# Optimization experiments

Measured on AMD Instinct MI355X. Metric: run time of the kernel, lower is better.

Reference implementation:

```python
import jax, jax.numpy as jnp
import numpy as np

N_NODES = 100000
N_EDGES = 1600000
IN_DIM = 512
HID_DIM = 64
N_CLASSES = 10
N_GRAPHS = 64


def setup_inputs() -> dict:
    key = jax.random.key(0)
    ks = jax.random.split(key, 8)
    x = jax.random.normal(ks[0], (N_NODES, IN_DIM), dtype=jnp.float32)
    edge_src = jax.random.randint(ks[1], (N_EDGES,), 0, N_NODES)
    edge_dst = jax.random.randint(ks[2], (N_EDGES,), 0, N_NODES)
    node2graph = jnp.sort(jax.random.randint(ks[3], (N_NODES,), 0, N_GRAPHS))
    W1 = jax.random.normal(ks[4], (IN_DIM, HID_DIM), dtype=jnp.float32) * (1.0 / np.sqrt(IN_DIM))
    b1 = jnp.zeros((HID_DIM,), dtype=jnp.float32)
    W2 = jax.random.normal(ks[5], (HID_DIM, N_CLASSES), dtype=jnp.float32) * (1.0 / np.sqrt(HID_DIM))
    b2 = jnp.zeros((N_CLASSES,), dtype=jnp.float32)
    return {"x": x, "edge_src": edge_src, "edge_dst": edge_dst,
            "node2graph": node2graph, "n_graphs": N_GRAPHS,
            "W1": W1, "b1": b1, "W2": W2, "b2": b2}


def reference(x, edge_src, edge_dst, node2graph, n_graphs, W1, b1, W2, b2):
    n = x.shape[0]
    ones_e = jnp.ones(edge_src.shape[0], dtype=x.dtype)
    # DGL GraphConv norm='both': src scaled by out-deg^-1/2, dst by in-deg^-1/2 (degrees clamped to 1)
    out_deg = jax.ops.segment_sum(ones_e, edge_src, num_segments=n)
    in_deg = jax.ops.segment_sum(ones_e, edge_dst, num_segments=n)
    src_norm = jax.lax.rsqrt(jnp.maximum(out_deg, 1.0))  # [N]
    dst_norm = jax.lax.rsqrt(jnp.maximum(in_deg, 1.0))   # [N]

    def graph_conv(h, W, b):
        h = (h * src_norm[:, None]) @ W                       # [N, out]
        agg = jax.ops.segment_sum(h[edge_src], edge_dst, num_segments=n)  # SpMM
        return agg * dst_norm[:, None] + b

    h = jax.nn.relu(graph_conv(x, W1, b1))
    h = graph_conv(h, W2, b2)
    # dgl.mean_nodes: per-graph mean over nodes
    counts = jax.ops.segment_sum(jnp.ones(n, dtype=x.dtype), node2graph, num_segments=n_graphs)
    sums = jax.ops.segment_sum(h, node2graph, num_segments=n_graphs)
    return sums / jnp.maximum(counts, 1.0)[:, None]
```

## Files before the change

kernel.cpp:

```cpp
#include <hip/hip_runtime.h>

#define NN 100000
#define NE 1600000
#define NG 64
#define BPB  50
#define NBUK 2000
#define NBUK2 2048
#define ECAP 1120
#define GPART 256
#define PREPB 128
#define ZEROB 3
#define GSTB ((NN+255)/256)

using bf16x8 = __attribute__((ext_vector_type(8))) short;
using f32x4  = __attribute__((ext_vector_type(4))) float;

__device__ inline unsigned short f2bf(float f){
    union { float f; unsigned u; } v; v.f = f;
    unsigned r = (v.u + 0x7FFFu + ((v.u >> 16) & 1u)) >> 16;
    return (unsigned short)r;
}

__device__ inline bf16x8 cvt8(float4 a, float4 b){
    union { unsigned u[4]; bf16x8 v; } r;
    asm("v_cvt_pk_bf16_f32 %0, %1, %2" : "=v"(r.u[0]) : "v"(a.x), "v"(a.y));
    asm("v_cvt_pk_bf16_f32 %0, %1, %2" : "=v"(r.u[1]) : "v"(a.z), "v"(a.w));
    asm("v_cvt_pk_bf16_f32 %0, %1, %2" : "=v"(r.u[2]) : "v"(b.x), "v"(b.y));
    asm("v_cvt_pk_bf16_f32 %0, %1, %2" : "=v"(r.u[3]) : "v"(b.z), "v"(b.w));
    return r.v;
}

__global__ __launch_bounds__(256) void k_start(const int* __restrict__ src, const int* __restrict__ dst,
                                               int* __restrict__ cntD, int* __restrict__ cntS, int E,
                                               const float* __restrict__ W1, short* __restrict__ Wb,
                                               float* __restrict__ pooled,
                                               const int* __restrict__ n2g, int* __restrict__ gstart, int N){
    __shared__ int hD[NBUK2], hS[NBUK2];
    int bid = blockIdx.x;
    int tid = threadIdx.x;
    if (bid < GPART){
        for (int i=tid; i<NBUK2; i+=256){ hD[i]=0; hS[i]=0; }
        __syncthreads();
        int chunk = (E + GPART - 1)/GPART;
        int start = bid*chunk;
        int end   = min(E, start + chunk);
        for (int e = start + tid; e < end; e += 256){
            atomicAdd(&hS[src[e]/BPB], 1);
            atomicAdd(&hD[dst[e]/BPB], 1);
        }
        __syncthreads();
        for (int i=tid; i<NBUK2; i+=256){
            cntD[bid*NBUK2 + i] = hD[i];
            cntS[bid*NBUK2 + i] = hS[i];
        }
    } else if (bid < GPART+PREPB){
        int i = (bid-GPART)*256 + tid;
        if (i < 512*64){
            int k = i >> 6, c = i & 63;
            int g = k >> 5, r = k & 31, s = r >> 3, j = r & 7;
            Wb[(((g*4+s)*64 + c) << 3) + j] = (short)f2bf(W1[i]);
        }
    } else if (bid < GPART+PREPB+ZEROB){
        int i = (bid-GPART-PREPB)*256 + tid;
        if (i < NG*10) pooled[i] = 0.f;
    } else {
        int n = (bid-GPART-PREPB-ZEROB)*256 + tid;
        if (n < N){
            int g  = n2g[n];
            int gp = (n == 0) ? -1 : n2g[n-1];
            if (gp != g){
                for (int gg = gp+1; gg <= g; ++gg) gstart[gg] = n;
            }
            if (n == N-1){
                for (int gg = g+1; gg <= NG; ++gg) gstart[gg] = N;
            }
        }
    }
}

__global__ __launch_bounds__(256) void k_scanA(const int* __restrict__ cntD, const int* __restrict__ cntS,
                                               int* __restrict__ totD, int* __restrict__ totS){
    int t = blockIdx.x*256 + threadIdx.x;
    int sD=0, sS=0;
    for (int b=0;b<GPART;b++){ sD += cntD[b*NBUK2+t]; sS += cntS[b*NBUK2+t]; }
    totD[t]=sD; totS[t]=sS;
}

__global__ __launch_bounds__(1024) void k_scanB(const int* __restrict__ totD, const int* __restrict__ totS,
                                                int* __restrict__ bstartD, int* __restrict__ bstartS){
    __shared__ int sd[1024];
    int t = threadIdx.x;
    {
        int v0 = totD[2*t], v1 = totD[2*t+1];
        sd[t] = v0+v1; __syncthreads();
        for (int off=1; off<1024; off<<=1){
            int tv = (t >= off) ? sd[t-off] : 0;
            __syncthreads();
            sd[t] += tv;
            __syncthreads();
        }
        int excl = sd[t] - v0 - v1;
        if (2*t   <= NBUK) bstartD[2*t]   = excl;
        if (2*t+1 <= NBUK) bstartD[2*t+1] = excl + v0;
        __syncthreads();
    }
    {
        int v0 = totS[2*t], v1 = totS[2*t+1];
        sd[t] = v0+v1; __syncthreads();
        for (int off=1; off<1024; off<<=1){
            int tv = (t >= off) ? sd[t-off] : 0;
            __syncthreads();
            sd[t] += tv;
            __syncthreads();
        }
        int excl = sd[t] - v0 - v1;
        if (2*t   <= NBUK) bstartS[2*t]   = excl;
        if (2*t+1 <= NBUK) bstartS[2*t+1] = excl + v0;
    }
}

__global__ __launch_bounds__(256) void k_scanC(int* __restrict__ cntD, int* __restrict__ cntS,
                                               const int* __restrict__ bstartD, const int* __restrict__ bstartS){
    int t = blockIdx.x*256 + threadIdx.x;
    if (t < NBUK){
        int rD = bstartD[t], rS = bstartS[t];
        for (int b=0;b<GPART;b++){
            int idx = b*NBUK2 + t;
            int o = cntD[idx]; cntD[idx] = rD; rD += o;
            o = cntS[idx];     cntS[idx] = rS; rS += o;
        }
    }
}

__global__ __launch_bounds__(256) void k_scatter(const int* __restrict__ src, const int* __restrict__ dst,
                                                 const int* __restrict__ cntD, const int* __restrict__ cntS,
                                                 int* __restrict__ pairs, int* __restrict__ srcl, int E){
    __shared__ unsigned oD[NBUK2], oS[NBUK2];
    for (int i=threadIdx.x; i<NBUK2; i+=256){
        oD[i] = (unsigned)cntD[blockIdx.x*NBUK2 + i];
        oS[i] = (unsigned)cntS[blockIdx.x*NBUK2 + i];
    }
    __syncthreads();
    int chunk = (E + GPART - 1)/GPART;
    int start = blockIdx.x*chunk;
    int end   = min(E, start + chunk);
    for (int e = start + threadIdx.x; e < end; e += 256){
        int s = src[e], d = dst[e];
        int bk = d/BPB;
        unsigned pD = atomicAdd(&oD[bk], 1u);
        pairs[pD] = (s << 6) | (d - bk*BPB);
        unsigned pS = atomicAdd(&oS[s/BPB], 1u);
        srcl[pS] = s;
    }
}

__global__ __launch_bounds__(256) void k_outdeg(const int* __restrict__ srcl, const int* __restrict__ bstartS,
                                                float* __restrict__ sn, int N){
    __shared__ int c[BPB];
    int b = blockIdx.x;
    if (threadIdx.x < BPB) c[threadIdx.x] = 0;
    __syncthreads();
    int s0 = bstartS[b], s1 = bstartS[b+1];
    int base = b*BPB;
    for (int i = s0 + threadIdx.x; i < s1; i += 256)
        atomicAdd(&c[srcl[i] - base], 1);
    __syncthreads();
    int node = base + threadIdx.x;
    if (threadIdx.x < BPB && node < N)
        sn[node] = rsqrtf((float)max(c[threadIdx.x], 1));
}

__global__ __launch_bounds__(256) void k_gemm1(const float* __restrict__ x, const short* __restrict__ Wb,
                                               const float* __restrict__ sn, unsigned short* __restrict__ hb, int N){
    const int lane = threadIdx.x & 63;
    const int wid  = threadIdx.x >> 6;
    const int rowBase = blockIdx.x*128 + wid*32;
    const int mrow = lane & 15;
    const int s    = lane >> 4;

    int rowA = rowBase + mrow;
    int rowB = rowBase + 16 + mrow;
    int rcA = (rowA < N) ? rowA : (N-1);
    int rcB = (rowB < N) ? rowB : (N-1);

    const float4* __restrict__ xv = (const float4*)x;
    const bf16x8* __restrict__ wv = (const bf16x8*)Wb;
    const float4* xrA = xv + (size_t)rcA*128 + s*2;
    const float4* xrB = xv + (size_t)rcB*128 + s*2;

    f32x4 accA0 = {0,0,0,0}, accA1 = {0,0,0,0}, accA2 = {0,0,0,0}, accA3 = {0,0,0,0};
    f32x4 accB0 = {0,0,0,0}, accB1 = {0,0,0,0}, accB2 = {0,0,0,0}, accB3 = {0,0,0,0};

    #pragma unroll 2
    for (int g=0; g<16; g++){
        float4 a0 = xrA[g*8 + 0];
        float4 a1 = xrA[g*8 + 1];
        float4 c0 = xrB[g*8 + 0];
        float4 c1 = xrB[g*8 + 1];
        bf16x8 afA = cvt8(a0, a1);
        bf16x8 afB = cvt8(c0, c1);
        int bbase = (g*4 + s)*64 + mrow;
        bf16x8 b0 = wv[bbase     ];
        bf16x8 b1 = wv[bbase + 16];
        bf16x8 b2 = wv[bbase + 32];
        bf16x8 b3 = wv[bbase + 48];
        accA0 = __builtin_amdgcn_mfma_f32_16x16x32_bf16(afA, b0, accA0, 0, 0, 0);
        accA1 = __builtin_amdgcn_mfma_f32_16x16x32_bf16(afA, b1, accA1, 0, 0, 0);
        accA2 = __builtin_amdgcn_mfma_f32_16x16x32_bf16(afA, b2, accA2, 0, 0, 0);
        accA3 = __builtin_amdgcn_mfma_f32_16x16x32_bf16(afA, b3, accA3, 0, 0, 0);
        accB0 = __builtin_amdgcn_mfma_f32_16x16x32_bf16(afB, b0, accB0, 0, 0, 0);
        accB1 = __builtin_amdgcn_mfma_f32_16x16x32_bf16(afB, b1, accB1, 0, 0, 0);
        accB2 = __builtin_amdgcn_mfma_f32_16x16x32_bf16(afB, b2, accB2, 0, 0, 0);
        accB3 = __builtin_amdgcn_mfma_f32_16x16x32_bf16(afB, b3, accB3, 0, 0, 0);
    }

    #pragma unroll
    for (int q=0; q<4; q++){
        int rr = rowBase + s*4 + q;
        if (rr < N){
            float scale = sn[rr];
            unsigned short* hp = hb + ((size_t)rr<<6) + mrow;
            hp[ 0] = f2bf(accA0[q] * scale);
            hp[16] = f2bf(accA1[q] * scale);
            hp[32] = f2bf(accA2[q] * scale);
            hp[48] = f2bf(accA3[q] * scale);
        }
        int r2 = rowBase + 16 + s*4 + q;
        if (r2 < N){
            float scale = sn[r2];
            unsigned short* hp = hb + ((size_t)r2<<6) + mrow;
            hp[ 0] = f2bf(accB0[q] * scale);
            hp[16] = f2bf(accB1[q] * scale);
            hp[32] = f2bf(accB2[q] * scale);
            hp[48] = f2bf(accB3[q] * scale);
        }
    }
}

__global__ __launch_bounds__(256) void k_agg(const int* __restrict__ pairs, const int* __restrict__ bstartD,
                                             const unsigned short* __restrict__ hb,
                                             const float* __restrict__ sn, const float* __restrict__ b1,
                                             const float* __restrict__ W2,
                                             float* __restrict__ h2, int* __restrict__ gsrc,
                                             int* __restrict__ glh, int N){
    __shared__ int lsrc[ECAP];
    __shared__ int lcnt[BPB];
    __shared__ int lstart[BPB+1];
    __shared__ unsigned lofs[BPB];
    __shared__ __align__(16) float w2t[10][64];
    __shared__ float b1s[64];
    __shared__ __align__(16) float a1s[BPB][68];
    int tid = threadIdx.x;
    if (tid < BPB) lcnt[tid] = 0;
    if (tid < 64)  b1s[tid] = b1[tid];
    for (int i=tid; i<640; i+=256){ int c = i>>6, k = i&63; w2t[c][k] = W2[k*10 + c]; }
    __syncthreads();

    int b = blockIdx.x;
    int nodeBase = b*BPB;
    int eb = bstartD[b], ee = bstartD[b+1];
    int ne = ee - eb;

    for (int i = tid; i < ne; i += 256){
        int pr = pairs[eb + i];
        atomicAdd(&lcnt[pr & 63], 1);
    }
    __syncthreads();
    if (tid < 64){
        int v = (tid < BPB) ? lcnt[tid] : 0;
        int sI = v;
        for (int off=1; off<64; off<<=1){
            int t = __shfl_up(sI, off);
            if (tid >= off) sI += t;
        }
        if (tid < BPB){
            lstart[tid] = sI - v;
            lofs[tid]   = (unsigned)(sI - v);
            if (tid == BPB-1) lstart[BPB] = sI;
        }
    }
    __syncthreads();
    for (int i = tid; i < ne; i += 256){
        int pr = pairs[eb + i];
        unsigned pos = atomicAdd(&lofs[pr & 63], 1u);
        lsrc[pos < ECAP ? pos : ECAP-1] = pr >> 6;
    }
    __syncthreads();

    for (int i = tid; i < ne; i += 256) gsrc[eb + i] = lsrc[i];
    if (tid <= BPB) glh[b*64 + tid] = eb + lstart[tid];

    int lane = tid & 63, wid = tid >> 6;
    int q  = lane >> 4;
    int c4 = lane & 15;

    for (int nl = wid; nl < BPB; nl += 4){
        int node = nodeBase + nl;
        int s0 = lstart[nl];
        int m  = lstart[nl+1] - s0;

        float a0=0.f, a1f=0.f, a2=0.f, a3=0.f;
        int j = 0;
        for (; j + 16 <= m; j += 16){
            int sa = lsrc[s0 + j + q];
            int sb = lsrc[s0 + j + 4 + q];
            int sc = lsrc[s0 + j + 8 + q];
            int sd = lsrc[s0 + j + 12 + q];
            uint2 va = *(const uint2*)(hb + ((size_t)sa<<6) + (c4<<2));
            uint2 vb = *(const uint2*)(hb + ((size_t)sb<<6) + (c4<<2));
            uint2 vc = *(const uint2*)(hb + ((size_t)sc<<6) + (c4<<2));
            uint2 vd = *(const uint2*)(hb + ((size_t)sd<<6) + (c4<<2));
            a0  += __uint_as_float((va.x & 0xffffu) << 16) + __uint_as_float((vb.x & 0xffffu) << 16)
                 + __uint_as_float((vc.x & 0xffffu) << 16) + __uint_as_float((vd.x & 0xffffu) << 16);
            a1f += __uint_as_float(va.x & 0xffff0000u) + __uint_as_float(vb.x & 0xffff0000u)
                 + __uint_as_float(vc.x & 0xffff0000u) + __uint_as_float(vd.x & 0xffff0000u);
            a2  += __uint_as_float((va.y & 0xffffu) << 16) + __uint_as_float((vb.y & 0xffffu) << 16)
                 + __uint_as_float((vc.y & 0xffffu) << 16) + __uint_as_float((vd.y & 0xffffu) << 16);
            a3  += __uint_as_float(va.y & 0xffff0000u) + __uint_as_float(vb.y & 0xffff0000u)
                 + __uint_as_float(vc.y & 0xffff0000u) + __uint_as_float(vd.y & 0xffff0000u);
        }
        for (; j + 8 <= m; j += 8){
            int sa = lsrc[s0 + j + q];
            int sb = lsrc[s0 + j + 4 + q];
            uint2 va = *(const uint2*)(hb + ((size_t)sa<<6) + (c4<<2));
            uint2 vb = *(const uint2*)(hb + ((size_t)sb<<6) + (c4<<2));
            a0  += __uint_as_float((va.x & 0xffffu) << 16) + __uint_as_float((vb.x & 0xffffu) << 16);
            a1f += __uint_as_float(va.x & 0xffff0000u) + __uint_as_float(vb.x & 0xffff0000u);
            a2  += __uint_as_float((va.y & 0xffffu) << 16) + __uint_as_float((vb.y & 0xffffu) << 16);
            a3  += __uint_as_float(va.y & 0xffff0000u) + __uint_as_float(vb.y & 0xffff0000u);
        }
        for (; j < m; j += 4){
            int idx = j + q;
            int idxc = (idx < m) ? idx : (m-1);
            int sa = lsrc[s0 + idxc];
            uint2 va = *(const uint2*)(hb + ((size_t)sa<<6) + (c4<<2));
            if (idx < m){
                a0  += __uint_as_float((va.x & 0xffffu) << 16);
                a1f += __uint_as_float(va.x & 0xffff0000u);
                a2  += __uint_as_float((va.y & 0xffffu) << 16);
                a3  += __uint_as_float(va.y & 0xffff0000u);
            }
        }
        a0  += __shfl_xor(a0, 16);  a0  += __shfl_xor(a0, 32);
        a1f += __shfl_xor(a1f, 16); a1f += __shfl_xor(a1f, 32);
        a2  += __shfl_xor(a2, 16);  a2  += __shfl_xor(a2, 32);
        a3  += __shfl_xor(a3, 16);  a3  += __shfl_xor(a3, 32);

        float dnv = rsqrtf((float)max(m, 1));
        float snv = sn[node];
        float r0 = fmaxf(fmaf(a0,  dnv, b1s[(c4<<2)+0]), 0.f) * snv;
        float r1 = fmaxf(fmaf(a1f, dnv, b1s[(c4<<2)+1]), 0.f) * snv;
        float r2 = fmaxf(fmaf(a2,  dnv, b1s[(c4<<2)+2]), 0.f) * snv;
        float r3 = fmaxf(fmaf(a3,  dnv, b1s[(c4<<2)+3]), 0.f) * snv;
        if (q == 0){
            *(float4*)(&a1s[nl][c4<<2]) = make_float4(r0, r1, r2, r3);
        }
    }
    __syncthreads();

    for (int i = tid; i < BPB*10; i += 256){
        int nl = i / 10;
        int c  = i - nl*10;
        int node = nodeBase + nl;
        if (node < N){
            const float4* ap = (const float4*)(&a1s[nl][0]);
            const float4* wp = (const float4*)(&w2t[c][0]);
            float acc = 0.f;
            #pragma unroll
            for (int p=0;p<16;p++){
                float4 a = ap[p]; float4 w = wp[p];
                acc = fmaf(a.x, w.x, fmaf(a.y, w.y, fmaf(a.z, w.z, fmaf(a.w, w.w, acc))));
            }
            h2[(size_t)node*10 + c] = acc;
        }
    }
}

__global__ __launch_bounds__(256) void k_pool2(const int* __restrict__ gsrc, const int* __restrict__ glh,
                                               const float* __restrict__ h2, const int* __restrict__ n2g,
                                               float* __restrict__ pooled, int N){
    __shared__ float accS[NG*10];
    int tid = threadIdx.x;
    for (int i=tid; i<NG*10; i+=256) accS[i] = 0.f;
    __syncthreads();
    int b = blockIdx.x;
    int nodeBase = b*BPB;
    int lane = tid & 63, wid = tid >> 6;
    int e6 = lane/10, c = lane - e6*10;
    bool active = (lane < 60);

    for (int nl = wid; nl < BPB; nl += 4){
        int node = nodeBase + nl;
        int base = glh[b*64 + nl];
        int m    = glh[b*64 + nl + 1] - base;
        float acc = 0.f;
        for (int j = 0; j < m; j += 6){
            int idx = j + e6;
            int idxc = (idx < m) ? idx : (m-1);
            int srcn = gsrc[base + idxc];
            float v = h2[(size_t)srcn*10 + c];
            if (active && idx < m) acc += v;
        }
        float t0 = __shfl(acc, lane+30); if (lane < 30) acc += t0;
        float t1 = __shfl(acc, lane+10);
        float t2 = __shfl(acc, lane+20);
        if (lane < 10){
            acc += t1 + t2;
            float dnv = rsqrtf((float)max(m, 1));
            int g = n2g[node];
            atomicAdd(&accS[g*10 + lane], dnv*acc);
        }
    }
    __syncthreads();
    int g0 = n2g[nodeBase], g1 = n2g[nodeBase + BPB - 1];
    int lo = g0*10, hi = g1*10 + 10;
    for (int i = lo + tid; i < hi; i += 256)
        atomicAdd(&pooled[i], accS[i]);
}

__global__ void k_out(const float* __restrict__ pooled, const int* __restrict__ gstart,
                      const float* __restrict__ b2, float* __restrict__ out){
    int i = blockIdx.x*blockDim.x + threadIdx.x;
    if (i < NG*10){
        int g = i/10, c = i - g*10;
        float cnt = (float)max(gstart[g+1] - gstart[g], 1);
        out[i] = pooled[i]/cnt + b2[c];
    }
}

extern "C" void kernel_launch(void* const* d_in, const int* in_sizes, int n_in,
                              void* d_out, int out_size, void* d_ws, size_t ws_size,
                              hipStream_t stream) {
    const float* x    = (const float*)d_in[0];
    const int*   esrc = (const int*)d_in[1];
    const int*   edst = (const int*)d_in[2];
    const int*   n2g  = (const int*)d_in[3];
    const float* W1   = (const float*)d_in[5];
    const float* b1   = (const float*)d_in[6];
    const float* W2   = (const float*)d_in[7];
    const float* b2   = (const float*)d_in[8];
    float* out = (float*)d_out;
    const int N = in_sizes[3];
    const int E = in_sizes[1];

    char* ws = (char*)d_ws;
    size_t off = 0;
    auto alloc = [&](size_t bytes) -> void* {
        void* p = ws + off;
        off = (off + bytes + 255) & ~(size_t)255;
        return p;
    };
    float* pooled  = (float*)alloc(NG*10*4);
    int*   cntD    = (int*)alloc((size_t)GPART*NBUK2*4);
    int*   cntS    = (int*)alloc((size_t)GPART*NBUK2*4);
    int*   totD    = (int*)alloc(NBUK2*4);
    int*   totS    = (int*)alloc(NBUK2*4);
    int*   bstartD = (int*)alloc((NBUK+1)*4);
    int*   bstartS = (int*)alloc((NBUK+1)*4);
    int*   pairs   = (int*)alloc((size_t)E*4);
    int*   srcl    = (int*)alloc((size_t)E*4);
    int*   gsrc    = (int*)alloc((size_t)E*4);
    int*   glh     = (int*)alloc((size_t)NBUK*64*4);
    float* sn      = (float*)alloc((size_t)N*4);
    int*   gstart  = (int*)alloc((size_t)(NG+1)*4);
    short* Wb      = (short*)alloc((size_t)512*64*2);
    unsigned short* hb = (unsigned short*)alloc((size_t)N*64*2);
    float* h2      = (float*)alloc((size_t)N*10*4);

    k_start<<<dim3(GPART+PREPB+ZEROB+GSTB), dim3(256), 0, stream>>>(
        esrc, edst, cntD, cntS, E, W1, Wb, pooled, n2g, gstart, N);
    k_scanA<<<dim3(8), dim3(256), 0, stream>>>(cntD, cntS, totD, totS);
    k_scanB<<<dim3(1), dim3(1024), 0, stream>>>(totD, totS, bstartD, bstartS);
    k_scanC<<<dim3(8), dim3(256), 0, stream>>>(cntD, cntS, bstartD, bstartS);
    k_scatter<<<dim3(GPART), dim3(256), 0, stream>>>(esrc, edst, cntD, cntS, pairs, srcl, E);
    k_outdeg<<<dim3(NBUK), dim3(256), 0, stream>>>(srcl, bstartS, sn, N);

    k_gemm1<<<dim3((N+127)/128), dim3(256), 0, stream>>>(x, Wb, sn, hb, N);

    k_agg<<<dim3(NBUK), dim3(256), 0, stream>>>(pairs, bstartD, hb, sn, b1, W2, h2, gsrc, glh, N);
    k_pool2<<<dim3(NBUK), dim3(256), 0, stream>>>(gsrc, glh, h2, n2g, pooled, N);
    k_out<<<dim3(3), dim3(256), 0, stream>>>(pooled, gstart, b2, out);
}
```

Measured before the change: 241.4 us.

## Slice bucket scans across more blocks, store src offsets as bytes, pad h2 rows

The column-wise scan over 256 partitions is split into 8 slices, so the count-reduction and offset-rewrite kernels run on 64 blocks instead of 8, each doing a shorter serial loop. A small scan kernel then combines the slice totals. The source list used for out-degree counting now stores a one-byte in-bucket offset instead of a 4-byte node id, which cuts scatter write traffic and outdeg read traffic. h2 rows are padded from 10 to 16 floats so the gathers in pooling are aligned, at the cost of more memory.

```diff
diff --git a/kernel.cpp b/kernel.cpp
--- a/kernel.cpp
+++ b/kernel.cpp
@@ -8,6 +8,8 @@
 #define NBUK2 2048
 #define ECAP 1120
 #define GPART 256
+#define NSLICE 8
+#define SLB (GPART/NSLICE)
 #define PREPB 128
 #define ZEROB 3
 #define GSTB ((NN+255)/256)
@@ -78,20 +80,26 @@
     }
 }
 
-__global__ __launch_bounds__(256) void k_scanA(const int* __restrict__ cntD, const int* __restrict__ cntS,
-                                               int* __restrict__ totD, int* __restrict__ totS){
-    int t = blockIdx.x*256 + threadIdx.x;
+__global__ __launch_bounds__(256) void k_scanCa(const int* __restrict__ cntD, const int* __restrict__ cntS,
+                                                int* __restrict__ sliceD, int* __restrict__ sliceS){
+    int id = blockIdx.x*256 + threadIdx.x;
+    int t = id & (NBUK2-1);
+    int s = id >> 11;
+    int b0 = s*SLB;
     int sD=0, sS=0;
-    for (int b=0;b<GPART;b++){ sD += cntD[b*NBUK2+t]; sS += cntS[b*NBUK2+t]; }
-    totD[t]=sD; totS[t]=sS;
-}
-
-__global__ __launch_bounds__(1024) void k_scanB(const int* __restrict__ totD, const int* __restrict__ totS,
+    for (int b=b0; b<b0+SLB; b++){ sD += cntD[b*NBUK2+t]; sS += cntS[b*NBUK2+t]; }
+    sliceD[s*NBUK2+t] = sD;
+    sliceS[s*NBUK2+t] = sS;
+}
+
+__global__ __launch_bounds__(1024) void k_scanB(const int* __restrict__ sliceD, const int* __restrict__ sliceS,
                                                 int* __restrict__ bstartD, int* __restrict__ bstartS){
     __shared__ int sd[1024];
     int t = threadIdx.x;
     {
-        int v0 = totD[2*t], v1 = totD[2*t+1];
+        int v0=0, v1=0;
+        #pragma unroll
+        for (int s=0;s<NSLICE;s++){ v0 += sliceD[s*NBUK2 + 2*t]; v1 += sliceD[s*NBUK2 + 2*t+1]; }
         sd[t] = v0+v1; __syncthreads();
         for (int off=1; off<1024; off<<=1){
             int tv = (t >= off) ? sd[t-off] : 0;
@@ -105,7 +113,9 @@
         __syncthreads();
     }
     {
-        int v0 = totS[2*t], v1 = totS[2*t+1];
+        int v0=0, v1=0;
+        #pragma unroll
+        for (int s=0;s<NSLICE;s++){ v0 += sliceS[s*NBUK2 + 2*t]; v1 += sliceS[s*NBUK2 + 2*t+1]; }
         sd[t] = v0+v1; __syncthreads();
         for (int off=1; off<1024; off<<=1){
             int tv = (t >= off) ? sd[t-off] : 0;
@@ -119,22 +129,26 @@
     }
 }
 
-__global__ __launch_bounds__(256) void k_scanC(int* __restrict__ cntD, int* __restrict__ cntS,
-                                               const int* __restrict__ bstartD, const int* __restrict__ bstartS){
-    int t = blockIdx.x*256 + threadIdx.x;
-    if (t < NBUK){
-        int rD = bstartD[t], rS = bstartS[t];
-        for (int b=0;b<GPART;b++){
-            int idx = b*NBUK2 + t;
-            int o = cntD[idx]; cntD[idx] = rD; rD += o;
-            o = cntS[idx];     cntS[idx] = rS; rS += o;
-        }
+__global__ __launch_bounds__(256) void k_scanCb(int* __restrict__ cntD, int* __restrict__ cntS,
+                                                const int* __restrict__ sliceD, const int* __restrict__ sliceS,
+                                                const int* __restrict__ bstartD, const int* __restrict__ bstartS){
+    int id = blockIdx.x*256 + threadIdx.x;
+    int t = id & (NBUK2-1);
+    int s = id >> 11;
+    if (t >= NBUK) return;
+    int rD = bstartD[t], rS = bstartS[t];
+    for (int sp=0; sp<s; sp++){ rD += sliceD[sp*NBUK2+t]; rS += sliceS[sp*NBUK2+t]; }
+    int b0 = s*SLB;
+    for (int b=b0; b<b0+SLB; b++){
+        int idx = b*NBUK2 + t;
+        int o = cntD[idx]; cntD[idx] = rD; rD += o;
+        o = cntS[idx];     cntS[idx] = rS; rS += o;
     }
 }
 
 __global__ __launch_bounds__(256) void k_scatter(const int* __restrict__ src, const int* __restrict__ dst,
                                                  const int* __restrict__ cntD, const int* __restrict__ cntS,
-                                                 int* __restrict__ pairs, int* __restrict__ srcl, int E){
+                                                 int* __restrict__ pairs, unsigned char* __restrict__ srcb, int E){
     __shared__ unsigned oD[NBUK2], oS[NBUK2];
     for (int i=threadIdx.x; i<NBUK2; i+=256){
         oD[i] = (unsigned)cntD[blockIdx.x*NBUK2 + i];
@@ -149,23 +163,24 @@
         int bk = d/BPB;
         unsigned pD = atomicAdd(&oD[bk], 1u);
         pairs[pD] = (s << 6) | (d - bk*BPB);
-        unsigned pS = atomicAdd(&oS[s/BPB], 1u);
-        srcl[pS] = s;
-    }
-}
-
-__global__ __launch_bounds__(256) void k_outdeg(const int* __restrict__ srcl, const int* __restrict__ bstartS,
+        int sb = s/BPB;
+        unsigned pS = atomicAdd(&oS[sb], 1u);
+        srcb[pS] = (unsigned char)(s - sb*BPB);
+    }
+}
+
+__global__ __launch_bounds__(256) void k_outdeg(const unsigned char* __restrict__ srcb,
+                                                const int* __restrict__ bstartS,
                                                 float* __restrict__ sn, int N){
     __shared__ int c[BPB];
     int b = blockIdx.x;
     if (threadIdx.x < BPB) c[threadIdx.x] = 0;
     __syncthreads();
     int s0 = bstartS[b], s1 = bstartS[b+1];
-    int base = b*BPB;
     for (int i = s0 + threadIdx.x; i < s1; i += 256)
-        atomicAdd(&c[srcl[i] - base], 1);
-    __syncthreads();
-    int node = base + threadIdx.x;
+        atomicAdd(&c[srcb[i]], 1);
+    __syncthreads();
+    int node = b*BPB + threadIdx.x;
     if (threadIdx.x < BPB && node < N)
         sn[node] = rsqrtf((float)max(c[threadIdx.x], 1));
 }
@@ -371,7 +386,7 @@
                 float4 a = ap[p]; float4 w = wp[p];
                 acc = fmaf(a.x, w.x, fmaf(a.y, w.y, fmaf(a.z, w.z, fmaf(a.w, w.w, acc))));
             }
-            h2[(size_t)node*10 + c] = acc;
+            h2[(size_t)node*16 + c] = acc;
         }
     }
 }
@@ -398,7 +413,7 @@
             int idx = j + e6;
             int idxc = (idx < m) ? idx : (m-1);
             int srcn = gsrc[base + idxc];
-            float v = h2[(size_t)srcn*10 + c];
+            float v = h2[(size_t)srcn*16 + c];
             if (active && idx < m) acc += v;
         }
         float t0 = __shfl(acc, lane+30); if (lane < 30) acc += t0;
@@ -453,27 +468,27 @@
     float* pooled  = (float*)alloc(NG*10*4);
     int*   cntD    = (int*)alloc((size_t)GPART*NBUK2*4);
     int*   cntS    = (int*)alloc((size_t)GPART*NBUK2*4);
-    int*   totD    = (int*)alloc(NBUK2*4);
-    int*   totS    = (int*)alloc(NBUK2*4);
+    int*   sliceD  = (int*)alloc((size_t)NSLICE*NBUK2*4);
+    int*   sliceS  = (int*)alloc((size_t)NSLICE*NBUK2*4);
     int*   bstartD = (int*)alloc((NBUK+1)*4);
     int*   bstartS = (int*)alloc((NBUK+1)*4);
     int*   pairs   = (int*)alloc((size_t)E*4);
-    int*   srcl    = (int*)alloc((size_t)E*4);
+    unsigned char* srcb = (unsigned char*)alloc((size_t)E);
     int*   gsrc    = (int*)alloc((size_t)E*4);
     int*   glh     = (int*)alloc((size_t)NBUK*64*4);
     float* sn      = (float*)alloc((size_t)N*4);
     int*   gstart  = (int*)alloc((size_t)(NG+1)*4);
     short* Wb      = (short*)alloc((size_t)512*64*2);
     unsigned short* hb = (unsigned short*)alloc((size_t)N*64*2);
-    float* h2      = (float*)alloc((size_t)N*10*4);
+    float* h2      = (float*)alloc((size_t)N*16*4);
 
     k_start<<<dim3(GPART+PREPB+ZEROB+GSTB), dim3(256), 0, stream>>>(
         esrc, edst, cntD, cntS, E, W1, Wb, pooled, n2g, gstart, N);
-    k_scanA<<<dim3(8), dim3(256), 0, stream>>>(cntD, cntS, totD, totS);
-    k_scanB<<<dim3(1), dim3(1024), 0, stream>>>(totD, totS, bstartD, bstartS);
-    k_scanC<<<dim3(8), dim3(256), 0, stream>>>(cntD, cntS, bstartD, bstartS);
-    k_scatter<<<dim3(GPART), dim3(256), 0, stream>>>(esrc, edst, cntD, cntS, pairs, srcl, E);
-    k_outdeg<<<dim3(NBUK), dim3(256), 0, stream>>>(srcl, bstartS, sn, N);
+    k_scanCa<<<dim3(64), dim3(256), 0, stream>>>(cntD, cntS, sliceD, sliceS);
+    k_scanB<<<dim3(1), dim3(1024), 0, stream>>>(sliceD, sliceS, bstartD, bstartS);
+    k_scanCb<<<dim3(64), dim3(256), 0, stream>>>(cntD, cntS, sliceD, sliceS, bstartD, bstartS);
+    k_scatter<<<dim3(GPART), dim3(256), 0, stream>>>(esrc, edst, cntD, cntS, pairs, srcb, E);
+    k_outdeg<<<dim3(NBUK), dim3(256), 0, stream>>>(srcb, bstartS, sn, N);
 
     k_gemm1<<<dim3((N+127)/128), dim3(256), 0, stream>>>(x, Wb, sn, hb, N);
 
```

Result: faster. 231.3 us (-4.2%).
